# Kernel tuning notes

Hardware: AMD Instinct MI355X
Metric: run time of the kernel (lower is better)

## Reference

```python
import jax, jax.numpy as jnp
import numpy as np

N_HEAD = 8
HIDDEN = 512
HEAD_DIM = HIDDEN // N_HEAD
EPS = 1e-5


def _layernorm(x, g, b):
    mu = jnp.mean(x, axis=-1, keepdims=True)
    var = jnp.var(x, axis=-1, keepdims=True)
    return (x - mu) * jax.lax.rsqrt(var + EPS) * g + b


def setup_inputs() -> dict:
    key = jax.random.key(0)
    ks = jax.random.split(key, 12)
    s = 1.0 / np.sqrt(HIDDEN)
    x = jax.random.normal(ks[0], (4, 2048, HIDDEN), dtype=jnp.float32)
    # per-head Q/K/V projections stacked: [H, D, dh] weights, [H, dh] biases
    Wq = jax.random.uniform(ks[1], (N_HEAD, HIDDEN, HEAD_DIM), minval=-s, maxval=s, dtype=jnp.float32)
    bq = jax.random.uniform(ks[2], (N_HEAD, HEAD_DIM), minval=-s, maxval=s, dtype=jnp.float32)
    Wk = jax.random.uniform(ks[3], (N_HEAD, HIDDEN, HEAD_DIM), minval=-s, maxval=s, dtype=jnp.float32)
    bk = jax.random.uniform(ks[4], (N_HEAD, HEAD_DIM), minval=-s, maxval=s, dtype=jnp.float32)
    Wv = jax.random.uniform(ks[5], (N_HEAD, HIDDEN, HEAD_DIM), minval=-s, maxval=s, dtype=jnp.float32)
    bv = jax.random.uniform(ks[6], (N_HEAD, HEAD_DIM), minval=-s, maxval=s, dtype=jnp.float32)
    Wm = jax.random.uniform(ks[7], (HIDDEN, HIDDEN), minval=-s, maxval=s, dtype=jnp.float32)
    bm = jax.random.uniform(ks[8], (HIDDEN,), minval=-s, maxval=s, dtype=jnp.float32)
    Wo = jax.random.uniform(ks[9], (HIDDEN, HIDDEN), minval=-s, maxval=s, dtype=jnp.float32)
    bo = jax.random.uniform(ks[10], (HIDDEN,), minval=-s, maxval=s, dtype=jnp.float32)
    g1 = jnp.ones((HIDDEN,), jnp.float32); b1 = jnp.zeros((HIDDEN,), jnp.float32)
    g2 = jnp.ones((HIDDEN,), jnp.float32); b2 = jnp.zeros((HIDDEN,), jnp.float32)
    return {"x": x, "g1": g1, "b1": b1, "Wq": Wq, "bq": bq, "Wk": Wk, "bk": bk,
            "Wv": Wv, "bv": bv, "Wm": Wm, "bm": bm, "g2": g2, "b2": b2, "Wo": Wo, "bo": bo}


def reference(x, g1, b1, Wq, bq, Wk, bk, Wv, bv, Wm, bm, g2, b2, Wo, bo):
    h = _layernorm(x, g1, b1)                                 # [B,S,D]
    # stacked per-head projections: [B,H,S,dh]
    q = jnp.einsum('bsd,hde->bhse', h, Wq) + bq[None, :, None, :]
    k = jnp.einsum('bsd,hde->bhse', h, Wk) + bk[None, :, None, :]
    v = jnp.einsum('bsd,hde->bhse', h, Wv) + bv[None, :, None, :]
    scores = jnp.einsum('bhse,bhte->bhst', q, k) / jnp.sqrt(jnp.float32(HEAD_DIM))
    attn = jax.nn.softmax(scores, axis=-1)                    # [B,H,S,S]
    out = jnp.einsum('bhst,bhte->bhse', attn, v)              # [B,H,S,dh]
    B, H, S, E = out.shape
    out_mha = jnp.transpose(out, (0, 2, 1, 3)).reshape(B, S, H * E)  # concat heads
    h_ln_post = out_mha @ Wm + bm + x
    h_fc = _layernorm(h_ln_post, g2, b2)
    return jax.nn.relu(h_fc @ Wo + bo) + h_ln_post
```

## Files before the change

kernel.cpp:

```cpp
#include <hip/hip_runtime.h>
#include <hip/hip_bf16.h>


typedef __attribute__((ext_vector_type(8))) short bf16x8;
typedef __attribute__((ext_vector_type(4))) float f32x4;
typedef __attribute__((ext_vector_type(16))) float f32x16;
typedef __attribute__((ext_vector_type(8))) unsigned short u16x8;

typedef union { bf16x8 v; unsigned u[4]; u16x8 s; } frag_u;

typedef const unsigned int __attribute__((address_space(1)))* gas_t;
typedef unsigned int __attribute__((address_space(3)))* las_t;
static __device__ __forceinline__ void glds16(const void* g, void* l) {
    __builtin_amdgcn_global_load_lds((gas_t)g, (las_t)l, 16, 0, 0);
}

static __device__ __forceinline__ unsigned short f2b(float f) {
    union { float f; unsigned u; } a; a.f = f;
    unsigned r = a.u + 0x7FFFu + ((a.u >> 16) & 1u);
    return (unsigned short)(r >> 16);
}
static __device__ __forceinline__ float b2f(unsigned short u) {
    union { unsigned u; float f; } c; c.u = ((unsigned)u) << 16; return c.f;
}
static __device__ __forceinline__ unsigned pack_bf16(float lo, float hi) {
    __hip_bfloat162 p = __float22bfloat162_rn(make_float2(lo, hi));
    unsigned r; __builtin_memcpy(&r, &p, 4); return r;
}
static __device__ __forceinline__ float fexp2(float x) {
#if __has_builtin(__builtin_amdgcn_exp2f)
    return __builtin_amdgcn_exp2f(x);
#else
    return exp2f(x);
#endif
}
static __device__ __forceinline__ void swap32(int hi, unsigned a, unsigned b,
                                              unsigned& x, unsigned& y) {
#if __has_builtin(__builtin_amdgcn_permlane32_swap)
    typedef __attribute__((ext_vector_type(2))) int i32x2;
    i32x2 r = __builtin_amdgcn_permlane32_swap((int)a, (int)b, false, false);
    x = (unsigned)r[0]; y = (unsigned)r[1];
#else
    unsigned ta = (unsigned)__shfl_xor((int)a, 32);
    unsigned tb = (unsigned)__shfl_xor((int)b, 32);
    x = hi ? tb : a;
    y = hi ? b : ta;
#endif
}

__global__ __launch_bounds__(256) void prep_weights_k(
    const float* __restrict__ Wq, const float* __restrict__ Wk, const float* __restrict__ Wv,
    const float* __restrict__ Wm, const float* __restrict__ Wo,
    unsigned short* __restrict__ wqT, unsigned short* __restrict__ wkT,
    unsigned short* __restrict__ wvT, unsigned short* __restrict__ wmT,
    unsigned short* __restrict__ woT)
{
    int idx = blockIdx.x * 256 + threadIdx.x;
    int n = idx >> 9, k = idx & 511;
    int h = n >> 6, e = n & 63;
    size_t src_qkv = ((size_t)h * 512 + k) * 64 + e;
    wqT[idx] = f2b(Wq[src_qkv]);
    wkT[idx] = f2b(Wk[src_qkv]);
    wvT[idx] = f2b(Wv[src_qkv]);
    wmT[idx] = f2b(Wm[(size_t)k * 512 + n]);
    woT[idx] = f2b(Wo[(size_t)k * 512 + n]);
}

__global__ __launch_bounds__(64) void ln_bf16_k(
    const float* __restrict__ X, const float* __restrict__ gam,
    const float* __restrict__ bet, unsigned short* __restrict__ O)
{
    int row = blockIdx.x, lane = threadIdx.x;
    const float4* xr = (const float4*)(X + (size_t)row * 512);
    float4 v0 = xr[lane * 2], v1 = xr[lane * 2 + 1];
    float vv[8] = {v0.x, v0.y, v0.z, v0.w, v1.x, v1.y, v1.z, v1.w};
    float s = 0.f, s2 = 0.f;
    #pragma unroll
    for (int j = 0; j < 8; ++j) { s += vv[j]; s2 += vv[j] * vv[j]; }
    #pragma unroll
    for (int d = 1; d < 64; d <<= 1) { s += __shfl_xor(s, d); s2 += __shfl_xor(s2, d); }
    float mean = s * (1.0f / 512.0f);
    float var  = s2 * (1.0f / 512.0f) - mean * mean;
    float rstd = rsqrtf(var + 1e-5f);
    int c = lane * 8;
    u16x8 o;
    #pragma unroll
    for (int j = 0; j < 8; ++j) o[j] = f2b((vv[j] - mean) * rstd * gam[c + j] + bet[c + j]);
    *(u16x8*)(O + (size_t)row * 512 + c) = o;
}

__global__ __launch_bounds__(256) void gemm_qkv_k(
    const unsigned short* __restrict__ A, const unsigned short* __restrict__ Bt,
    const float* __restrict__ bq, const float* __restrict__ bk, const float* __restrict__ bv,
    unsigned short* __restrict__ Qo, unsigned short* __restrict__ Ko,
    unsigned short* __restrict__ VtO)
{
    __shared__ unsigned short Al[128 * 32];
    __shared__ unsigned short Bl[128 * 32];
    int tid = threadIdx.x;
    int wid = tid >> 6, lane = tid & 63;
    int lr = lane & 15, lg = lane >> 4;
    int m0 = blockIdx.x * 128, n0 = blockIdx.y * 128;
    int seg = blockIdx.y >> 2;
    int wr = (wid >> 1) * 64, wc = (wid & 1) * 64;
    f32x4 acc[4][4] = {};
    const unsigned short* Ag = A  + (size_t)(m0 + wid * 32 + (lane >> 2)) * 512 + (lane & 3) * 8;
    const unsigned short* Bg = Bt + (size_t)(n0 + wid * 32 + (lane >> 2)) * 512 + (lane & 3) * 8;
    unsigned short* Alw = Al + wid * 32 * 32;
    unsigned short* Blw = Bl + wid * 32 * 32;
    for (int k0 = 0; k0 < 512; k0 += 32) {
        __syncthreads();
        glds16(Ag + k0,             Alw);
        glds16(Ag + k0 + 16 * 512,  Alw + 16 * 32);
        glds16(Bg + k0,             Blw);
        glds16(Bg + k0 + 16 * 512,  Blw + 16 * 32);
        __syncthreads();
        bf16x8 af[4], bfr[4];
        #pragma unroll
        for (int m = 0; m < 4; ++m) af[m]  = *(const bf16x8*)(Al + (wr + m * 16 + lr) * 32 + lg * 8);
        #pragma unroll
        for (int n = 0; n < 4; ++n) bfr[n] = *(const bf16x8*)(Bl + (wc + n * 16 + lr) * 32 + lg * 8);
        #pragma unroll
        for (int m = 0; m < 4; ++m)
            #pragma unroll
            for (int n = 0; n < 4; ++n)
                acc[m][n] = __builtin_amdgcn_mfma_f32_16x16x32_bf16(af[m], bfr[n], acc[m][n], 0, 0, 0);
    }
    const float* bb = seg == 0 ? bq : (seg == 1 ? bk : bv);
    unsigned short* dst = seg == 0 ? Qo : Ko;
    #pragma unroll
    for (int m = 0; m < 4; ++m)
      #pragma unroll
      for (int n = 0; n < 4; ++n) {
        int gr0 = m0 + wr + m * 16 + 4 * lg;
        int nc  = ((blockIdx.y & 3) << 7) + wc + n * 16 + lr;
        float bias = bb[nc];
        if (seg < 2) {
            #pragma unroll
            for (int j = 0; j < 4; ++j)
                dst[(size_t)(gr0 + j) * 512 + nc] = f2b(acc[m][n][j] + bias);
        } else {
            int bbk = gr0 >> 11, ss = gr0 & 2047, hh = nc >> 6, ee = nc & 63;
            ushort4 pv;
            pv.x = f2b(acc[m][n][0] + bias);
            pv.y = f2b(acc[m][n][1] + bias);
            pv.z = f2b(acc[m][n][2] + bias);
            pv.w = f2b(acc[m][n][3] + bias);
            *(ushort4*)&VtO[((size_t)((bbk * 8 + hh) * 64 + ee) << 11) + ss] = pv;
        }
      }
}

template<int MODE>
__global__ __launch_bounds__(256) void gemm_n64_k(
    const unsigned short* __restrict__ A, const unsigned short* __restrict__ Bt,
    const float* __restrict__ bias, const float* __restrict__ aux,
    float* __restrict__ Cout)
{
    __shared__ unsigned short Al[128 * 32];
    __shared__ unsigned short Bl[64 * 32];
    int tid = threadIdx.x;
    int wid = tid >> 6, lane = tid & 63;
    int lr = lane & 15, lg = lane >> 4;
    int m0 = blockIdx.x * 128, n0 = blockIdx.y * 64;
    int wr = wid * 32;
    f32x4 acc[2][4] = {};
    const unsigned short* Ag = A  + (size_t)(m0 + wid * 32 + (lane >> 2)) * 512 + (lane & 3) * 8;
    const unsigned short* Bg = Bt + (size_t)(n0 + wid * 16 + (lane >> 2)) * 512 + (lane & 3) * 8;
    unsigned short* Alw = Al + wid * 32 * 32;
    unsigned short* Blw = Bl + wid * 16 * 32;
    for (int k0 = 0; k0 < 512; k0 += 32) {
        __syncthreads();
        glds16(Ag + k0,            Alw);
        glds16(Ag + k0 + 16 * 512, Alw + 16 * 32);
        glds16(Bg + k0,            Blw);
        __syncthreads();
        bf16x8 af[2], bfr[4];
        #pragma unroll
        for (int m = 0; m < 2; ++m) af[m]  = *(const bf16x8*)(Al + (wr + m * 16 + lr) * 32 + lg * 8);
        #pragma unroll
        for (int n = 0; n < 4; ++n) bfr[n] = *(const bf16x8*)(Bl + (n * 16 + lr) * 32 + lg * 8);
        #pragma unroll
        for (int m = 0; m < 2; ++m)
            #pragma unroll
            for (int n = 0; n < 4; ++n)
                acc[m][n] = __builtin_amdgcn_mfma_f32_16x16x32_bf16(af[m], bfr[n], acc[m][n], 0, 0, 0);
    }
    #pragma unroll
    for (int m = 0; m < 2; ++m)
      #pragma unroll
      for (int n = 0; n < 4; ++n)
        #pragma unroll
        for (int j = 0; j < 4; ++j) {
            int gr = m0 + wr + m * 16 + 4 * lg + j;
            int gc = n0 + n * 16 + lr;
            float v = acc[m][n][j] + bias[gc];
            if (MODE == 3) v = v > 0.0f ? v : 0.0f;
            Cout[(size_t)gr * 512 + gc] = v + aux[(size_t)gr * 512 + gc];
        }
}

__global__ __launch_bounds__(128) void attn12_k(
    const unsigned short* __restrict__ Q, const unsigned short* __restrict__ K,
    const unsigned short* __restrict__ Vt, unsigned short* __restrict__ O)
{
    __shared__ __align__(16) unsigned short KlA[4096], KlB[4096];
    __shared__ __align__(16) unsigned short VlA[4096], VlB[4096];

    const int tid  = threadIdx.x;
    const int lane = tid & 63;
    const int q31  = lane & 31;
    const int hi   = lane >> 5;
    const int wid  = tid >> 6;

    int bid = blockIdx.x;
    int xcd = bid & 7, idx = bid >> 3;
    int bh  = xcd + 8 * (idx >> 5);
    int qt  = idx & 31;
    int b = bh >> 3, h = bh & 7;
    int q0 = qt * 64 + wid * 32;

    const unsigned short* Qb = Q  + (size_t)b * 2048 * 512 + h * 64;
    const unsigned short* Kb = K  + (size_t)b * 2048 * 512 + h * 64;
    const unsigned short* Vb = Vt + (size_t)(b * 8 + h) * 64 * 2048;

    frag_u qf[4];
    const float qs = 0.125f * 1.44269504f;
    #pragma unroll
    for (int ds = 0; ds < 4; ++ds) {
        u16x8 raw = *(const u16x8*)(Qb + (size_t)(q0 + q31) * 512 + ds * 16 + hi * 8);
        #pragma unroll
        for (int i = 0; i < 4; ++i)
            qf[ds].u[i] = pack_bf16(b2f(raw[2 * i]) * qs, b2f(raw[2 * i + 1]) * qs);
    }

    frag_u onesf;
    #pragma unroll
    for (int i = 0; i < 4; ++i) onesf.u[i] = 0x3F803F80u;

    unsigned soff[8];
    #pragma unroll
    for (int j = 0; j < 8; ++j) {
        int row31 = j * 4 + (lane >> 4);
        int x = (lane & 15) ^ (row31 & 15);
        int t = 32 * (x >> 3) + row31;
        int s = x & 7;
        soff[j] = (wid == 0) ? (unsigned)(t * 512 + s * 8)
                             : (unsigned)(t * 2048 + s * 8);
    }
    const unsigned short* Gb = (wid == 0) ? Kb : Vb;

    auto STAGE = [&](unsigned short* buf, int t0) {
        const unsigned short* g = Gb + (wid == 0 ? (size_t)t0 * 512 : (size_t)t0);
        #pragma unroll
        for (int j = 0; j < 8; ++j)
            glds16(g + soff[j], buf + j * 512);
    };

    f32x16 acc0, acc1, lacc;
    #pragma unroll
    for (int r = 0; r < 16; ++r) { acc0[r] = 0.0f; acc1[r] = 0.0f; lacc[r] = 0.0f; }
    const int swz = (q31 & 15) << 4;

    auto COMPUTE = [&](const unsigned short* Kh_, const unsigned short* Vh_) {
        const char* Kh = (const char*)Kh_;
        const char* Vh = (const char*)Vh_;
        f32x16 s0, s1;
        #pragma unroll
        for (int r = 0; r < 16; ++r) { s0[r] = 0.0f; s1[r] = 0.0f; }
        __builtin_amdgcn_s_setprio(1);
        #pragma unroll
        for (int ds = 0; ds < 4; ++ds) {
            bf16x8 k0 = *(const bf16x8*)(Kh + q31 * 256 + ((ds * 32 + hi * 16) ^ swz));
            bf16x8 k1 = *(const bf16x8*)(Kh + q31 * 256 + ((128 + ds * 32 + hi * 16) ^ swz));
            s0 = __builtin_amdgcn_mfma_f32_32x32x16_bf16(k0, qf[ds].v, s0, 0, 0, 0);
            s1 = __builtin_amdgcn_mfma_f32_32x32x16_bf16(k1, qf[ds].v, s1, 0, 0, 0);
        }
        __builtin_amdgcn_s_setprio(0);

        #pragma unroll
        for (int r = 0; r < 16; ++r) {
            s0[r] = fexp2(s0[r]);
            s1[r] = fexp2(s1[r]);
        }

        frag_u pa[4];
        #pragma unroll
        for (int g = 0; g < 2; ++g) {
            unsigned A0 = pack_bf16(s0[8 * g + 0], s0[8 * g + 1]);
            unsigned A1 = pack_bf16(s0[8 * g + 2], s0[8 * g + 3]);
            unsigned A2 = pack_bf16(s0[8 * g + 4], s0[8 * g + 5]);
            unsigned A3 = pack_bf16(s0[8 * g + 6], s0[8 * g + 7]);
            swap32(hi, A0, A2, pa[g].u[0], pa[g].u[2]);
            swap32(hi, A1, A3, pa[g].u[1], pa[g].u[3]);
            unsigned B0 = pack_bf16(s1[8 * g + 0], s1[8 * g + 1]);
            unsigned B1 = pack_bf16(s1[8 * g + 2], s1[8 * g + 3]);
            unsigned B2 = pack_bf16(s1[8 * g + 4], s1[8 * g + 5]);
            unsigned B3 = pack_bf16(s1[8 * g + 6], s1[8 * g + 7]);
            swap32(hi, B0, B2, pa[2 + g].u[0], pa[2 + g].u[2]);
            swap32(hi, B1, B3, pa[2 + g].u[1], pa[2 + g].u[3]);
        }

        __builtin_amdgcn_s_setprio(1);
        #pragma unroll
        for (int ks = 0; ks < 4; ++ks) {
            bf16x8 v0 = *(const bf16x8*)(Vh + q31 * 256 + ((ks * 32 + hi * 16) ^ swz));
            bf16x8 v1 = *(const bf16x8*)(Vh + q31 * 256 + ((128 + ks * 32 + hi * 16) ^ swz));
            acc0 = __builtin_amdgcn_mfma_f32_32x32x16_bf16(pa[ks].v, v0, acc0, 0, 0, 0);
            acc1 = __builtin_amdgcn_mfma_f32_32x32x16_bf16(pa[ks].v, v1, acc1, 0, 0, 0);
            lacc = __builtin_amdgcn_mfma_f32_32x32x16_bf16(pa[ks].v, onesf.v, lacc, 0, 0, 0);
        }
        __builtin_amdgcn_s_setprio(0);
    };

    STAGE(wid == 0 ? KlA : VlA, 0);
    __syncthreads();

    #pragma unroll 1
    for (int it = 0; it < 32; it += 2) {
        if (it + 1 < 32) STAGE(wid == 0 ? KlB : VlB, (it + 1) * 64);
        COMPUTE(KlA, VlA);
        __syncthreads();
        if (it + 2 < 32) STAGE(wid == 0 ? KlA : VlA, (it + 2) * 64);
        COMPUTE(KlB, VlB);
        __syncthreads();
    }

    #pragma unroll
    for (int r = 0; r < 16; ++r) {
        int cr = (r & 3) + 8 * (r >> 2) + 4 * hi;
        float li = 1.0f / lacc[r];
        size_t rowoff = (size_t)(b * 2048 + q0 + cr) * 512 + h * 64 + q31;
        O[rowoff]      = f2b(acc0[r] * li);
        O[rowoff + 32] = f2b(acc1[r] * li);
    }
}

extern "C" void kernel_launch(void* const* d_in, const int* in_sizes, int n_in,
                              void* d_out, int out_size, void* d_ws, size_t ws_size,
                              hipStream_t stream)
{
    const float* x  = (const float*)d_in[0];
    const float* g1 = (const float*)d_in[1];
    const float* b1 = (const float*)d_in[2];
    const float* Wq = (const float*)d_in[3];
    const float* bq = (const float*)d_in[4];
    const float* Wk = (const float*)d_in[5];
    const float* bk = (const float*)d_in[6];
    const float* Wv = (const float*)d_in[7];
    const float* bv = (const float*)d_in[8];
    const float* Wm = (const float*)d_in[9];
    const float* bm = (const float*)d_in[10];
    const float* g2 = (const float*)d_in[11];
    const float* b2 = (const float*)d_in[12];
    const float* Wo = (const float*)d_in[13];
    const float* bo = (const float*)d_in[14];
    float* out = (float*)d_out;

    char* ws = (char*)d_ws;
    const size_t EB = (size_t)8192 * 512 * 2;
    unsigned short* h1  = (unsigned short*)(ws);
    unsigned short* qb  = (unsigned short*)(ws + EB);
    unsigned short* kb  = (unsigned short*)(ws + 2 * EB);
    unsigned short* vtb = (unsigned short*)(ws + 3 * EB);
    unsigned short* ao  = (unsigned short*)(ws + 4 * EB);
    unsigned short* h2  = (unsigned short*)(ws + 5 * EB);
    float*          hlp = (float*)(ws + 6 * EB);
    unsigned short* wqT = (unsigned short*)(ws + 8 * EB);
    unsigned short* wkT = wqT + 512 * 512;
    unsigned short* wvT = wkT + 512 * 512;
    unsigned short* wmT = wvT + 512 * 512;
    unsigned short* woT = wmT + 512 * 512;

    prep_weights_k<<<1024, 256, 0, stream>>>(Wq, Wk, Wv, Wm, Wo, wqT, wkT, wvT, wmT, woT);
    ln_bf16_k<<<8192, 64, 0, stream>>>(x, g1, b1, h1);
    gemm_qkv_k<<<dim3(64, 12), 256, 0, stream>>>(h1, wqT, bq, bk, bv, qb, kb, vtb);
    attn12_k<<<1024, 128, 0, stream>>>(qb, kb, vtb, ao);
    gemm_n64_k<2><<<dim3(64, 8), 256, 0, stream>>>(ao, wmT, bm, x, hlp);
    ln_bf16_k<<<8192, 64, 0, stream>>>(hlp, g2, b2, h2);
    gemm_n64_k<3><<<dim3(64, 8), 256, 0, stream>>>(h2, woT, bo, hlp, out);
}
```

Baseline: 133.4 us.

## Give each attention wave private double-buffered K/V staging and drop block barriers

The attention kernel no longer splits staging so that wave 0 loads K and wave 1 loads V into shared buffers. Instead, each wave loads both K and V tiles into its own double-buffered region of a 64 KB LDS allocation. Block-wide __syncthreads are replaced by per-wave s_waitcnt vmcnt waits and scheduling barriers, so the two waves no longer stall on each other. In exchange, each wave issues twice the global-to-LDS traffic, per-block LDS grows from 32 KB to 64 KB (which may limit resident blocks per CU), and the last iteration prefetches a wasted wrapped-around tile.

Result: slower. 147.7 us (+10.7%).

```diff
diff --git a/kernel.cpp b/kernel.cpp
--- a/kernel.cpp
+++ b/kernel.cpp
@@ -200,12 +200,11 @@
         }
 }
 
-__global__ __launch_bounds__(128) void attn12_k(
+__global__ __launch_bounds__(128) void attn13_k(
     const unsigned short* __restrict__ Q, const unsigned short* __restrict__ K,
     const unsigned short* __restrict__ Vt, unsigned short* __restrict__ O)
 {
-    __shared__ __align__(16) unsigned short KlA[4096], KlB[4096];
-    __shared__ __align__(16) unsigned short VlA[4096], VlB[4096];
+    __shared__ __align__(16) char smem[65536];
 
     const int tid  = threadIdx.x;
     const int lane = tid & 63;
@@ -238,23 +237,30 @@
     #pragma unroll
     for (int i = 0; i < 4; ++i) onesf.u[i] = 0x3F803F80u;
 
-    unsigned soff[8];
+    unsigned kof[8], vof[8];
     #pragma unroll
     for (int j = 0; j < 8; ++j) {
         int row31 = j * 4 + (lane >> 4);
         int x = (lane & 15) ^ (row31 & 15);
         int t = 32 * (x >> 3) + row31;
         int s = x & 7;
-        soff[j] = (wid == 0) ? (unsigned)(t * 512 + s * 8)
-                             : (unsigned)(t * 2048 + s * 8);
-    }
-    const unsigned short* Gb = (wid == 0) ? Kb : Vb;
-
-    auto STAGE = [&](unsigned short* buf, int t0) {
-        const unsigned short* g = Gb + (wid == 0 ? (size_t)t0 * 512 : (size_t)t0);
-        #pragma unroll
-        for (int j = 0; j < 8; ++j)
-            glds16(g + soff[j], buf + j * 512);
+        kof[j] = (unsigned)(t * 512 + s * 8);
+        vof[j] = (unsigned)(t * 2048 + s * 8);
+    }
+
+    char* base = smem + wid * 32768;
+    unsigned short* KA = (unsigned short*)(base);
+    unsigned short* KB = (unsigned short*)(base + 8192);
+    unsigned short* VA = (unsigned short*)(base + 16384);
+    unsigned short* VB = (unsigned short*)(base + 24576);
+
+    auto STAGE = [&](unsigned short* kb_, unsigned short* vb_, int t0) {
+        const unsigned short* gk = Kb + (size_t)t0 * 512;
+        const unsigned short* gv = Vb + t0;
+        #pragma unroll
+        for (int j = 0; j < 8; ++j) glds16(gk + kof[j], kb_ + j * 512);
+        #pragma unroll
+        for (int j = 0; j < 8; ++j) glds16(gv + vof[j], vb_ + j * 512);
     };
 
     f32x16 acc0, acc1, lacc;
@@ -313,18 +319,19 @@
         __builtin_amdgcn_s_setprio(0);
     };
 
-    STAGE(wid == 0 ? KlA : VlA, 0);
-    __syncthreads();
-
+    STAGE(KA, VA, 0);
     #pragma unroll 1
     for (int it = 0; it < 32; it += 2) {
-        if (it + 1 < 32) STAGE(wid == 0 ? KlB : VlB, (it + 1) * 64);
-        COMPUTE(KlA, VlA);
-        __syncthreads();
-        if (it + 2 < 32) STAGE(wid == 0 ? KlA : VlA, (it + 2) * 64);
-        COMPUTE(KlB, VlB);
-        __syncthreads();
-    }
+        STAGE(KB, VB, (it + 1) * 64);
+        asm volatile("s_waitcnt vmcnt(16)" ::: "memory");
+        __builtin_amdgcn_sched_barrier(0);
+        COMPUTE(KA, VA);
+        STAGE(KA, VA, ((it + 2) & 31) * 64);
+        asm volatile("s_waitcnt vmcnt(16)" ::: "memory");
+        __builtin_amdgcn_sched_barrier(0);
+        COMPUTE(KB, VB);
+    }
+    asm volatile("s_waitcnt vmcnt(0)" ::: "memory");
 
     #pragma unroll
     for (int r = 0; r < 16; ++r) {
@@ -375,7 +382,7 @@
     prep_weights_k<<<1024, 256, 0, stream>>>(Wq, Wk, Wv, Wm, Wo, wqT, wkT, wvT, wmT, woT);
     ln_bf16_k<<<8192, 64, 0, stream>>>(x, g1, b1, h1);
     gemm_qkv_k<<<dim3(64, 12), 256, 0, stream>>>(h1, wqT, bq, bk, bv, qb, kb, vtb);
-    attn12_k<<<1024, 128, 0, stream>>>(qb, kb, vtb, ao);
+    attn13_k<<<1024, 128, 0, stream>>>(qb, kb, vtb, ao);
     gemm_n64_k<2><<<dim3(64, 8), 256, 0, stream>>>(ao, wmT, bm, x, hlp);
     ln_bf16_k<<<8192, 64, 0, stream>>>(hlp, g2, b2, h2);
     gemm_n64_k<3><<<dim3(64, 8), 256, 0, stream>>>(h2, woT, bo, hlp, out);
```

## Double-buffer GEMM LDS staging and merge weight prep with first layernorm

Applied to the files above, without the earlier changes.

Both GEMM kernels now use two LDS buffers so the async global-to-LDS load of the next K-slice is issued before computing the current one. This is meant to hide load latency behind the MFMA work. The weight-conversion and first layernorm kernels are merged into one launch, and layernorm now processes four rows per 256-thread block to cut launch and small-block overhead. The cost is twice the LDS per GEMM block, which may reduce occupancy.

After: 130.7 us. 1.02x faster.

```diff
diff --git a/kernel.cpp b/kernel.cpp
--- a/kernel.cpp
+++ b/kernel.cpp
@@ -48,29 +48,11 @@
 #endif
 }
 
-__global__ __launch_bounds__(256) void prep_weights_k(
-    const float* __restrict__ Wq, const float* __restrict__ Wk, const float* __restrict__ Wv,
-    const float* __restrict__ Wm, const float* __restrict__ Wo,
-    unsigned short* __restrict__ wqT, unsigned short* __restrict__ wkT,
-    unsigned short* __restrict__ wvT, unsigned short* __restrict__ wmT,
-    unsigned short* __restrict__ woT)
-{
-    int idx = blockIdx.x * 256 + threadIdx.x;
-    int n = idx >> 9, k = idx & 511;
-    int h = n >> 6, e = n & 63;
-    size_t src_qkv = ((size_t)h * 512 + k) * 64 + e;
-    wqT[idx] = f2b(Wq[src_qkv]);
-    wkT[idx] = f2b(Wk[src_qkv]);
-    wvT[idx] = f2b(Wv[src_qkv]);
-    wmT[idx] = f2b(Wm[(size_t)k * 512 + n]);
-    woT[idx] = f2b(Wo[(size_t)k * 512 + n]);
-}
-
-__global__ __launch_bounds__(64) void ln_bf16_k(
+static __device__ __forceinline__ void ln_row(
     const float* __restrict__ X, const float* __restrict__ gam,
-    const float* __restrict__ bet, unsigned short* __restrict__ O)
-{
-    int row = blockIdx.x, lane = threadIdx.x;
+    const float* __restrict__ bet, unsigned short* __restrict__ O,
+    int row, int lane)
+{
     const float4* xr = (const float4*)(X + (size_t)row * 512);
     float4 v0 = xr[lane * 2], v1 = xr[lane * 2 + 1];
     float vv[8] = {v0.x, v0.y, v0.z, v0.w, v1.x, v1.y, v1.z, v1.w};
@@ -89,14 +71,48 @@
     *(u16x8*)(O + (size_t)row * 512 + c) = o;
 }
 
+__global__ __launch_bounds__(256) void prep_ln_k(
+    const float* __restrict__ Wq, const float* __restrict__ Wk, const float* __restrict__ Wv,
+    const float* __restrict__ Wm, const float* __restrict__ Wo,
+    unsigned short* __restrict__ wqT, unsigned short* __restrict__ wkT,
+    unsigned short* __restrict__ wvT, unsigned short* __restrict__ wmT,
+    unsigned short* __restrict__ woT,
+    const float* __restrict__ X, const float* __restrict__ g1,
+    const float* __restrict__ b1, unsigned short* __restrict__ h1)
+{
+    int bx = blockIdx.x;
+    if (bx < 1024) {
+        int idx = bx * 256 + threadIdx.x;
+        int n = idx >> 9, k = idx & 511;
+        int h = n >> 6, e = n & 63;
+        size_t src_qkv = ((size_t)h * 512 + k) * 64 + e;
+        wqT[idx] = f2b(Wq[src_qkv]);
+        wkT[idx] = f2b(Wk[src_qkv]);
+        wvT[idx] = f2b(Wv[src_qkv]);
+        wmT[idx] = f2b(Wm[(size_t)k * 512 + n]);
+        woT[idx] = f2b(Wo[(size_t)k * 512 + n]);
+    } else {
+        int row = (bx - 1024) * 4 + (threadIdx.x >> 6);
+        ln_row(X, g1, b1, h1, row, threadIdx.x & 63);
+    }
+}
+
+__global__ __launch_bounds__(256) void ln4_k(
+    const float* __restrict__ X, const float* __restrict__ gam,
+    const float* __restrict__ bet, unsigned short* __restrict__ O)
+{
+    int row = blockIdx.x * 4 + (threadIdx.x >> 6);
+    ln_row(X, gam, bet, O, row, threadIdx.x & 63);
+}
+
 __global__ __launch_bounds__(256) void gemm_qkv_k(
     const unsigned short* __restrict__ A, const unsigned short* __restrict__ Bt,
     const float* __restrict__ bq, const float* __restrict__ bk, const float* __restrict__ bv,
     unsigned short* __restrict__ Qo, unsigned short* __restrict__ Ko,
     unsigned short* __restrict__ VtO)
 {
-    __shared__ unsigned short Al[128 * 32];
-    __shared__ unsigned short Bl[128 * 32];
+    __shared__ unsigned short Al[2][128 * 32];
+    __shared__ unsigned short Bl[2][128 * 32];
     int tid = threadIdx.x;
     int wid = tid >> 6, lane = tid & 63;
     int lr = lane & 15, lg = lane >> 4;
@@ -106,26 +122,38 @@
     f32x4 acc[4][4] = {};
     const unsigned short* Ag = A  + (size_t)(m0 + wid * 32 + (lane >> 2)) * 512 + (lane & 3) * 8;
     const unsigned short* Bg = Bt + (size_t)(n0 + wid * 32 + (lane >> 2)) * 512 + (lane & 3) * 8;
-    unsigned short* Alw = Al + wid * 32 * 32;
-    unsigned short* Blw = Bl + wid * 32 * 32;
-    for (int k0 = 0; k0 < 512; k0 += 32) {
-        __syncthreads();
-        glds16(Ag + k0,             Alw);
-        glds16(Ag + k0 + 16 * 512,  Alw + 16 * 32);
-        glds16(Bg + k0,             Blw);
-        glds16(Bg + k0 + 16 * 512,  Blw + 16 * 32);
-        __syncthreads();
+    const int lofs = wid * 32 * 32;
+
+    auto STAGE = [&](int buf, int k0) {
+        glds16(Ag + k0,            Al[buf] + lofs);
+        glds16(Ag + k0 + 16 * 512, Al[buf] + lofs + 16 * 32);
+        glds16(Bg + k0,            Bl[buf] + lofs);
+        glds16(Bg + k0 + 16 * 512, Bl[buf] + lofs + 16 * 32);
+    };
+    auto COMPUTE = [&](int buf) {
         bf16x8 af[4], bfr[4];
         #pragma unroll
-        for (int m = 0; m < 4; ++m) af[m]  = *(const bf16x8*)(Al + (wr + m * 16 + lr) * 32 + lg * 8);
-        #pragma unroll
-        for (int n = 0; n < 4; ++n) bfr[n] = *(const bf16x8*)(Bl + (wc + n * 16 + lr) * 32 + lg * 8);
+        for (int m = 0; m < 4; ++m) af[m]  = *(const bf16x8*)(Al[buf] + (wr + m * 16 + lr) * 32 + lg * 8);
+        #pragma unroll
+        for (int n = 0; n < 4; ++n) bfr[n] = *(const bf16x8*)(Bl[buf] + (wc + n * 16 + lr) * 32 + lg * 8);
         #pragma unroll
         for (int m = 0; m < 4; ++m)
             #pragma unroll
             for (int n = 0; n < 4; ++n)
                 acc[m][n] = __builtin_amdgcn_mfma_f32_16x16x32_bf16(af[m], bfr[n], acc[m][n], 0, 0, 0);
-    }
+    };
+
+    STAGE(0, 0);
+    #pragma unroll 1
+    for (int k0 = 0; k0 < 512; k0 += 64) {
+        __syncthreads();
+        if (k0 + 32 < 512) STAGE(1, k0 + 32);
+        COMPUTE(0);
+        __syncthreads();
+        if (k0 + 64 < 512) STAGE(0, k0 + 64);
+        COMPUTE(1);
+    }
+
     const float* bb = seg == 0 ? bq : (seg == 1 ? bk : bv);
     unsigned short* dst = seg == 0 ? Qo : Ko;
     #pragma unroll
@@ -157,8 +185,8 @@
     const float* __restrict__ bias, const float* __restrict__ aux,
     float* __restrict__ Cout)
 {
-    __shared__ unsigned short Al[128 * 32];
-    __shared__ unsigned short Bl[64 * 32];
+    __shared__ unsigned short Al[2][128 * 32];
+    __shared__ unsigned short Bl[2][64 * 32];
     int tid = threadIdx.x;
     int wid = tid >> 6, lane = tid & 63;
     int lr = lane & 15, lg = lane >> 4;
@@ -167,25 +195,38 @@
     f32x4 acc[2][4] = {};
     const unsigned short* Ag = A  + (size_t)(m0 + wid * 32 + (lane >> 2)) * 512 + (lane & 3) * 8;
     const unsigned short* Bg = Bt + (size_t)(n0 + wid * 16 + (lane >> 2)) * 512 + (lane & 3) * 8;
-    unsigned short* Alw = Al + wid * 32 * 32;
-    unsigned short* Blw = Bl + wid * 16 * 32;
-    for (int k0 = 0; k0 < 512; k0 += 32) {
-        __syncthreads();
-        glds16(Ag + k0,            Alw);
-        glds16(Ag + k0 + 16 * 512, Alw + 16 * 32);
-        glds16(Bg + k0,            Blw);
-        __syncthreads();
+    const int aofs = wid * 32 * 32;
+    const int bofs = wid * 16 * 32;
+
+    auto STAGE = [&](int buf, int k0) {
+        glds16(Ag + k0,            Al[buf] + aofs);
+        glds16(Ag + k0 + 16 * 512, Al[buf] + aofs + 16 * 32);
+        glds16(Bg + k0,            Bl[buf] + bofs);
+    };
+    auto COMPUTE = [&](int buf) {
         bf16x8 af[2], bfr[4];
         #pragma unroll
-        for (int m = 0; m < 2; ++m) af[m]  = *(const bf16x8*)(Al + (wr + m * 16 + lr) * 32 + lg * 8);
-        #pragma unroll
-        for (int n = 0; n < 4; ++n) bfr[n] = *(const bf16x8*)(Bl + (n * 16 + lr) * 32 + lg * 8);
+        for (int m = 0; m < 2; ++m) af[m]  = *(const bf16x8*)(Al[buf] + (wr + m * 16 + lr) * 32 + lg * 8);
+        #pragma unroll
+        for (int n = 0; n < 4; ++n) bfr[n] = *(const bf16x8*)(Bl[buf] + (n * 16 + lr) * 32 + lg * 8);
         #pragma unroll
         for (int m = 0; m < 2; ++m)
             #pragma unroll
             for (int n = 0; n < 4; ++n)
                 acc[m][n] = __builtin_amdgcn_mfma_f32_16x16x32_bf16(af[m], bfr[n], acc[m][n], 0, 0, 0);
-    }
+    };
+
+    STAGE(0, 0);
+    #pragma unroll 1
+    for (int k0 = 0; k0 < 512; k0 += 64) {
+        __syncthreads();
+        if (k0 + 32 < 512) STAGE(1, k0 + 32);
+        COMPUTE(0);
+        __syncthreads();
+        if (k0 + 64 < 512) STAGE(0, k0 + 64);
+        COMPUTE(1);
+    }
+
     #pragma unroll
     for (int m = 0; m < 2; ++m)
       #pragma unroll
@@ -372,11 +413,12 @@
     unsigned short* wmT = wvT + 512 * 512;
     unsigned short* woT = wmT + 512 * 512;
 
-    prep_weights_k<<<1024, 256, 0, stream>>>(Wq, Wk, Wv, Wm, Wo, wqT, wkT, wvT, wmT, woT);
-    ln_bf16_k<<<8192, 64, 0, stream>>>(x, g1, b1, h1);
+    prep_ln_k<<<3072, 256, 0, stream>>>(Wq, Wk, Wv, Wm, Wo,
+                                        wqT, wkT, wvT, wmT, woT,
+                                        x, g1, b1, h1);
     gemm_qkv_k<<<dim3(64, 12), 256, 0, stream>>>(h1, wqT, bq, bk, bv, qb, kb, vtb);
     attn12_k<<<1024, 128, 0, stream>>>(qb, kb, vtb, ao);
     gemm_n64_k<2><<<dim3(64, 8), 256, 0, stream>>>(ao, wmT, bm, x, hlp);
-    ln_bf16_k<<<8192, 64, 0, stream>>>(hlp, g2, b2, h2);
+    ln4_k<<<2048, 256, 0, stream>>>(hlp, g2, b2, h2);
     gemm_n64_k<3><<<dim3(64, 8), 256, 0, stream>>>(h2, woT, bo, hlp, out);
 }
```
